# Performance work log

Hardware: AMD Instinct MI355X
Metric: run time of the kernel (lower is better)

## Reference

```python
import jax, jax.numpy as jnp
import numpy as np

BN_EPS = 1e-3  # keras BatchNormalization default epsilon


def setup_inputs() -> dict:
    key = jax.random.key(0)
    ks = jax.random.split(key, 8)
    B, N, F = 4, 512, 64
    C = 2 * F + 1  # concat(adj[...,1], feat_i[...,F], feat_j[...,F])
    return {
        "node_features": jax.random.normal(ks[0], (B, N, F), dtype=jnp.float32),
        "adjacency": jax.random.uniform(ks[1], (B, N, N), dtype=jnp.float32),
        "gamma": jnp.ones((C,), dtype=jnp.float32),
        "beta": jnp.zeros((C,), dtype=jnp.float32),
        "moving_mean": jax.random.normal(ks[2], (C,), dtype=jnp.float32) * 0.1,
        "moving_var": jax.random.uniform(ks[3], (C,), dtype=jnp.float32) + 0.5,
        "conv_w": jax.random.normal(ks[4], (C,), dtype=jnp.float32) / np.sqrt(C),
        "conv_b": jnp.zeros((1,), dtype=jnp.float32),
    }


def reference(node_features, adjacency, gamma, beta, moving_mean, moving_var, conv_w, conv_b):
    B, N, F = node_features.shape
    # augment_adjacency_matrix: pairwise broadcast of node features + adjacency channel
    adj = adjacency[..., None]                                        # [B,N,N,1]
    feat_i = jnp.broadcast_to(node_features[:, :, None, :], (B, N, N, F))  # row-tiled
    feat_j = jnp.broadcast_to(node_features[:, None, :, :], (B, N, N, F))  # col-tiled
    aug = jnp.concatenate([adj, feat_i, feat_j], axis=-1)             # [B,N,N,2F+1]
    # BnActConv(1, 1): BN (inference stats) -> ReLU -> 1x1 Conv2D with 1 filter
    inv = gamma * jax.lax.rsqrt(moving_var + BN_EPS)
    x = aug * inv + (beta - moving_mean * inv)
    x = jax.nn.relu(x)
    out = jnp.einsum("bijc,c->bij", x, conv_w) + conv_b[0]           # [B,N,N]
    return out
```

## Files before the change

kernel.cpp:

```cpp
#include <hip/hip_runtime.h>

#define BN_EPS 1e-3f

__global__ void node_sums_kernel(const float* __restrict__ feat,
                                 const float* __restrict__ gamma,
                                 const float* __restrict__ beta,
                                 const float* __restrict__ mean,
                                 const float* __restrict__ var,
                                 const float* __restrict__ w,
                                 float* __restrict__ Si,
                                 float* __restrict__ Sj,
                                 int F) {
    const int row = blockIdx.x;
    const int f   = threadIdx.x;
    const float x = feat[(long long)row * F + f];

    const int ci = 1 + f;
    const int cj = 1 + F + f;

    const float invi = gamma[ci] * rsqrtf(var[ci] + BN_EPS);
    const float bi   = beta[ci] - mean[ci] * invi;
    const float invj = gamma[cj] * rsqrtf(var[cj] + BN_EPS);
    const float bj   = beta[cj] - mean[cj] * invj;

    float vi = fmaxf(fmaf(x, invi, bi), 0.0f) * w[ci];
    float vj = fmaxf(fmaf(x, invj, bj), 0.0f) * w[cj];

    #pragma unroll
    for (int off = 32; off > 0; off >>= 1) {
        vi += __shfl_down(vi, off, 64);
        vj += __shfl_down(vj, off, 64);
    }
    if (f == 0) {
        Si[row] = vi;
        Sj[row] = vj;
    }
}

__global__ void out_kernel(const float* __restrict__ adj,
                           const float* __restrict__ Si,
                           const float* __restrict__ Sj,
                           float* __restrict__ out,
                           const float* __restrict__ gamma,
                           const float* __restrict__ beta,
                           const float* __restrict__ mean,
                           const float* __restrict__ var,
                           const float* __restrict__ w,
                           const float* __restrict__ conv_b,
                           int N, int total4) {
    const int t = blockIdx.x * blockDim.x + threadIdx.x;
    if (t >= total4) return;

    const float inv0 = gamma[0] * rsqrtf(var[0] + BN_EPS);
    const float b0   = beta[0] - mean[0] * inv0;
    const float w0   = w[0];
    const float cb   = conv_b[0];

    const float4 a = reinterpret_cast<const float4*>(adj)[t];

    const int idx = t * 4;
    const int row = idx / N;
    const int b   = row / N;
    const int j0  = idx - row * N;

    const float si = Si[row] + cb;
    const float* sjp = Sj + b * N + j0;

    float4 r;
    r.x = fmaxf(fmaf(a.x, inv0, b0), 0.0f) * w0 + si + sjp[0];
    r.y = fmaxf(fmaf(a.y, inv0, b0), 0.0f) * w0 + si + sjp[1];
    r.z = fmaxf(fmaf(a.z, inv0, b0), 0.0f) * w0 + si + sjp[2];
    r.w = fmaxf(fmaf(a.w, inv0, b0), 0.0f) * w0 + si + sjp[3];

    reinterpret_cast<float4*>(out)[t] = r;
}

extern "C" void kernel_launch(void* const* d_in, const int* in_sizes, int n_in,
                              void* d_out, int out_size, void* d_ws, size_t ws_size,
                              hipStream_t stream) {
    const float* feat  = (const float*)d_in[0];
    const float* adj   = (const float*)d_in[1];
    const float* gamma = (const float*)d_in[2];
    const float* beta  = (const float*)d_in[3];
    const float* mean  = (const float*)d_in[4];
    const float* var   = (const float*)d_in[5];
    const float* w     = (const float*)d_in[6];
    const float* cb    = (const float*)d_in[7];

    const int C  = in_sizes[2];
    const int F  = (C - 1) / 2;
    const int BN = in_sizes[0] / F;
    const long long total = in_sizes[1];
    const int N  = (int)(total / BN);

    float* Si = (float*)d_ws;
    float* Sj = Si + BN;

    node_sums_kernel<<<BN, F, 0, stream>>>(feat, gamma, beta, mean, var, w, Si, Sj, F);

    const int total4  = (int)(total / 4);
    const int threads = 256;
    const int blocks  = (total4 + threads - 1) / threads;
    out_kernel<<<blocks, threads, 0, stream>>>(adj, Si, Sj, (float*)d_out,
                                               gamma, beta, mean, var, w, cb,
                                               N, total4);
}
```

Measured before the change: 12.14 us.

## Fuse node-sum and output kernels into one with per-block Sj recompute

Merges the two launches into a single kernel where each block handles 8 rows of one batch. Each block recomputes the column sums Sj for all nodes of its batch into shared memory, plus its own row sums, then writes the outputs. This removes a launch and the global workspace round-trip, at the cost of redundantly recomputing all Sj values in every block and doing a serial prologue before the streaming phase.

```diff
diff --git a/kernel.cpp b/kernel.cpp
--- a/kernel.cpp
+++ b/kernel.cpp
@@ -1,78 +1,106 @@
 #include <hip/hip_runtime.h>
 
 #define BN_EPS 1e-3f
+#define RPB   8
+#define MAXN  512
+#define MAXF  64
 
-__global__ void node_sums_kernel(const float* __restrict__ feat,
-                                 const float* __restrict__ gamma,
-                                 const float* __restrict__ beta,
-                                 const float* __restrict__ mean,
-                                 const float* __restrict__ var,
-                                 const float* __restrict__ w,
-                                 float* __restrict__ Si,
-                                 float* __restrict__ Sj,
-                                 int F) {
-    const int row = blockIdx.x;
-    const int f   = threadIdx.x;
-    const float x = feat[(long long)row * F + f];
+__global__ __launch_bounds__(256) void fused_kernel(
+    const float* __restrict__ feat,
+    const float* __restrict__ adj,
+    const float* __restrict__ gamma,
+    const float* __restrict__ beta,
+    const float* __restrict__ mean,
+    const float* __restrict__ var,
+    const float* __restrict__ w,
+    const float* __restrict__ conv_b,
+    float* __restrict__ out,
+    int N, int F)
+{
+    __shared__ float sInvI[MAXF], sBi[MAXF], sWi[MAXF];
+    __shared__ float sInvJ[MAXF], sBj[MAXF], sWj[MAXF];
+    __shared__ float Sj_l[MAXN];
+    __shared__ float Si_l[RPB];
 
-    const int ci = 1 + f;
-    const int cj = 1 + F + f;
+    const int tid = threadIdx.x;
+    const int bpb = N / RPB;
+    const int b   = blockIdx.x / bpb;
+    const int i0  = (blockIdx.x - b * bpb) * RPB;
 
-    const float invi = gamma[ci] * rsqrtf(var[ci] + BN_EPS);
-    const float bi   = beta[ci] - mean[ci] * invi;
-    const float invj = gamma[cj] * rsqrtf(var[cj] + BN_EPS);
-    const float bj   = beta[cj] - mean[cj] * invj;
+    if (tid < F) {
+        const int ci = 1 + tid, cj = 1 + F + tid;
+        const float gi = gamma[ci] * rsqrtf(var[ci] + BN_EPS);
+        sInvI[tid] = gi;
+        sBi[tid]   = beta[ci] - mean[ci] * gi;
+        sWi[tid]   = w[ci];
+        const float gj = gamma[cj] * rsqrtf(var[cj] + BN_EPS);
+        sInvJ[tid] = gj;
+        sBj[tid]   = beta[cj] - mean[cj] * gj;
+        sWj[tid]   = w[cj];
+    }
+    __syncthreads();
 
-    float vi = fmaxf(fmaf(x, invi, bi), 0.0f) * w[ci];
-    float vj = fmaxf(fmaf(x, invj, bj), 0.0f) * w[cj];
+    const float* fb = feat + (long long)b * N * F;
 
-    #pragma unroll
-    for (int off = 32; off > 0; off >>= 1) {
-        vi += __shfl_down(vi, off, 64);
-        vj += __shfl_down(vj, off, 64);
+    for (int r = tid; r < N; r += blockDim.x) {
+        const float4* fr = reinterpret_cast<const float4*>(fb + (long long)r * F);
+        float acc = 0.f;
+        #pragma unroll
+        for (int f4 = 0; f4 < (MAXF >> 2); ++f4) {
+            if (f4 >= (F >> 2)) break;
+            const float4 x  = fr[f4];
+            const float4 iv = reinterpret_cast<const float4*>(sInvJ)[f4];
+            const float4 bb = reinterpret_cast<const float4*>(sBj)[f4];
+            const float4 ww = reinterpret_cast<const float4*>(sWj)[f4];
+            acc += fmaxf(fmaf(x.x, iv.x, bb.x), 0.f) * ww.x;
+            acc += fmaxf(fmaf(x.y, iv.y, bb.y), 0.f) * ww.y;
+            acc += fmaxf(fmaf(x.z, iv.z, bb.z), 0.f) * ww.z;
+            acc += fmaxf(fmaf(x.w, iv.w, bb.w), 0.f) * ww.w;
+        }
+        Sj_l[r] = acc;
     }
-    if (f == 0) {
-        Si[row] = vi;
-        Sj[row] = vj;
+
+    {
+        const int wv = tid >> 6, ln = tid & 63;
+        for (int k = wv; k < RPB; k += (256 >> 6)) {
+            const int r = i0 + k;
+            float v = 0.f;
+            if (ln < F) {
+                const float x = fb[(long long)r * F + ln];
+                v = fmaxf(fmaf(x, sInvI[ln], sBi[ln]), 0.f) * sWi[ln];
+            }
+            #pragma unroll
+            for (int off = 32; off > 0; off >>= 1)
+                v += __shfl_down(v, off, 64);
+            if (ln == 0) Si_l[k] = v;
+        }
     }
-}
-
-__global__ void out_kernel(const float* __restrict__ adj,
-                           const float* __restrict__ Si,
-                           const float* __restrict__ Sj,
-                           float* __restrict__ out,
-                           const float* __restrict__ gamma,
-                           const float* __restrict__ beta,
-                           const float* __restrict__ mean,
-                           const float* __restrict__ var,
-                           const float* __restrict__ w,
-                           const float* __restrict__ conv_b,
-                           int N, int total4) {
-    const int t = blockIdx.x * blockDim.x + threadIdx.x;
-    if (t >= total4) return;
+    __syncthreads();
 
     const float inv0 = gamma[0] * rsqrtf(var[0] + BN_EPS);
     const float b0   = beta[0] - mean[0] * inv0;
     const float w0   = w[0];
     const float cb   = conv_b[0];
 
-    const float4 a = reinterpret_cast<const float4*>(adj)[t];
+    const int il  = tid >> 5;
+    const int l32 = tid & 31;
+    const long long rowbase = ((long long)b * N + i0 + il) * N;
+    const float4* arow = reinterpret_cast<const float4*>(adj + rowbase);
+    float4*       orow = reinterpret_cast<float4*>(out + rowbase);
+    const float4* sj4  = reinterpret_cast<const float4*>(Sj_l);
+    const float   si   = Si_l[il] + cb;
 
-    const int idx = t * 4;
-    const int row = idx / N;
-    const int b   = row / N;
-    const int j0  = idx - row * N;
-
-    const float si = Si[row] + cb;
-    const float* sjp = Sj + b * N + j0;
-
-    float4 r;
-    r.x = fmaxf(fmaf(a.x, inv0, b0), 0.0f) * w0 + si + sjp[0];
-    r.y = fmaxf(fmaf(a.y, inv0, b0), 0.0f) * w0 + si + sjp[1];
-    r.z = fmaxf(fmaf(a.z, inv0, b0), 0.0f) * w0 + si + sjp[2];
-    r.w = fmaxf(fmaf(a.w, inv0, b0), 0.0f) * w0 + si + sjp[3];
-
-    reinterpret_cast<float4*>(out)[t] = r;
+    const int n4 = N >> 2;
+    for (int j4 = l32; j4 < n4; j4 += 32) {
+        const float4 a = arow[j4];
+        const float4 s = sj4[j4];
+        float4 r;
+        r.x = fmaxf(fmaf(a.x, inv0, b0), 0.f) * w0 + si + s.x;
+        r.y = fmaxf(fmaf(a.y, inv0, b0), 0.f) * w0 + si + s.y;
+        r.z = fmaxf(fmaf(a.z, inv0, b0), 0.f) * w0 + si + s.z;
+        r.w = fmaxf(fmaf(a.w, inv0, b0), 0.f) * w0 + si + s.w;
+        orow[j4] = r;
+    }
 }
 
 extern "C" void kernel_launch(void* const* d_in, const int* in_sizes, int n_in,
@@ -92,16 +120,10 @@
     const int BN = in_sizes[0] / F;
     const long long total = in_sizes[1];
     const int N  = (int)(total / BN);
+    const int B  = BN / N;
 
-    float* Si = (float*)d_ws;
-    float* Sj = Si + BN;
+    const int blocks = B * (N / RPB);
 
-    node_sums_kernel<<<BN, F, 0, stream>>>(feat, gamma, beta, mean, var, w, Si, Sj, F);
-
-    const int total4  = (int)(total / 4);
-    const int threads = 256;
-    const int blocks  = (total4 + threads - 1) / threads;
-    out_kernel<<<blocks, threads, 0, stream>>>(adj, Si, Sj, (float*)d_out,
-                                               gamma, beta, mean, var, w, cb,
-                                               N, total4);
+    fused_kernel<<<blocks, 256, 0, stream>>>(feat, adj, gamma, beta, mean, var,
+                                             w, cb, (float*)d_out, N, F);
 }
```

After: 12.68 us. 1.04x slower.
